# Kernel tuning notes

Measured on AMD Instinct MI355X. Metric: run time of the kernel, lower is better.

## Reference

```python
import jax, jax.numpy as jnp
import numpy as np

EPS = 1e-5


def _adabin_act_quant_1bit(x):
    # AdabinQuantizer, num_bits=1, layerwise=False, beta=0 (fresh zeros param).
    # alpha: per-sample scale, detached: 2*mean|x - beta| / sqrt(Qp=1), shape (N,1,1,1)
    alpha = jax.lax.stop_gradient(2.0 * jnp.mean(jnp.abs(x), axis=(1, 2, 3), keepdims=True))
    alpha = jnp.maximum(alpha, EPS)
    # forward: alpha * sign(x); STE grad: pass-through where |x/alpha| <= 1 (clip grad)
    clipped = jnp.clip(x / alpha, -1.0, 1.0)
    return alpha * (clipped + jax.lax.stop_gradient(jnp.sign(x) - clipped))


def _bwn_weight_quant(w):
    # BwnQuantizer, layerwise=False: per-output-channel L1 mean scale,
    # w_q = sign(w) * m, STE backward = identity.
    m = jnp.mean(jnp.abs(w), axis=(1, 2, 3), keepdims=True)  # (O,1,1,1)
    return w + jax.lax.stop_gradient(jnp.sign(w) * m - w)


def setup_inputs() -> dict:
    key = jax.random.key(0)
    kx, kw = jax.random.split(key)
    x = jax.random.normal(kx, (32, 256, 56, 56), dtype=jnp.float32)
    weight = jax.random.normal(kw, (256, 256, 3, 3), dtype=jnp.float32) * 0.05
    return {"x": x, "weight": weight}


def reference(x, weight):
    xq = _adabin_act_quant_1bit(x)
    wq = _bwn_weight_quant(weight)
    out = jax.lax.conv_general_dilated(
        xq, wq,
        window_strides=(1, 1),
        padding=((1, 1), (1, 1)),
        dimension_numbers=("NCHW", "OIHW", "NCHW"),
    )
    return out
```

## Files before the change

kernel.cpp:

```cpp
#include <hip/hip_runtime.h>
#include <cstdint>

typedef int   i32x4 __attribute__((ext_vector_type(4)));
typedef int   i32x8 __attribute__((ext_vector_type(8)));
typedef float f32x4 __attribute__((ext_vector_type(4)));

static constexpr int N_IMG = 32, HWP = 3136, KK = 2304, HP = 58;
static constexpr size_t XPAD_BYTES = (size_t)N_IMG * HP * HP * 256;
static constexpr size_t OFF_XPAD = 0;
static constexpr size_t OFF_WSGN = XPAD_BYTES;
static constexpr size_t OFF_MSC  = OFF_WSGN + (size_t)256 * KK;
static constexpr size_t OFF_ACC  = OFF_MSC + 1024;

__device__ __forceinline__ void async16(const void* g, const void* l) {
    __builtin_amdgcn_global_load_lds(
        (const __attribute__((address_space(1))) uint32_t*)g,
        (__attribute__((address_space(3))) uint32_t*)l, 16, 0, 0);
}

__device__ __forceinline__ unsigned char sign_fp8(float v) {
    return (v > 0.f) ? 0x38u : ((v < 0.f) ? 0xB8u : 0u);
}

__device__ __forceinline__ int xoff(int kt) {
    int rs = kt >> 1, rr = rs / 3, ss = rs - rr * 3;
    return (rr * HP + ss) * 256 + ((kt & 1) << 7);
}

__global__ __launch_bounds__(256) void k_wm(const float* __restrict__ w,
                                            unsigned char* __restrict__ wA,
                                            float* __restrict__ msc,
                                            float* __restrict__ acc32) {
    int ko = blockIdx.x, t = threadIdx.x;
    __shared__ unsigned char s[2304];
    __shared__ float red[4];
    float sum = 0.f;
    #pragma unroll
    for (int i = 0; i < 9; ++i) {
        float v = w[(size_t)ko * KK + i * 256 + t];
        sum += fabsf(v);
        s[i * 256 + t] = sign_fp8(v);
    }
    #pragma unroll
    for (int off = 32; off; off >>= 1) sum += __shfl_down(sum, off, 64);
    if ((t & 63) == 0) red[t >> 6] = sum;
    __syncthreads();
    if (t == 0) msc[ko] = (red[0] + red[1] + red[2] + red[3]) * (1.f / 2304.f);
    if (ko == 0 && t < 32) acc32[t] = 0.f;
    #pragma unroll
    for (int i = 0; i < 9; ++i)
        wA[((size_t)(i * 2 + (t >> 7)) * 256 + ko) * 128 + (t & 127)] = s[t * 9 + i];
}

__global__ __launch_bounds__(256) void k_xpad(const float* __restrict__ x,
                                              unsigned char* __restrict__ xpad,
                                              float* __restrict__ acc32) {
    int bx = blockIdx.x, n = blockIdx.y;
    int t = threadIdx.x;
    {
        int g = (n * 49 + bx) * 256 + t;
        if (g < 32 * 228 * 16) {
            int n2 = g / 3648, rem = g - n2 * 3648;
            int pos = rem >> 4, j = rem & 15;
            int h, wq;
            if (pos < 58)       { h = 0;         wq = pos; }
            else if (pos < 116) { h = 57;        wq = pos - 58; }
            else if (pos < 172) { h = pos - 115; wq = 0; }
            else                { h = pos - 171; wq = 57; }
            *(i32x4*)&xpad[(((size_t)n2 * HP + h) * HP + wq) * 256 + j * 16] =
                (i32x4){0, 0, 0, 0};
        }
    }
    int hw0 = bx * 64;
    int cg = t & 15, hwg = t >> 4;
    int c16 = cg * 16;
    int hwb = hw0 + hwg * 4;

    f32x4 v[16];
    #pragma unroll
    for (int jc = 0; jc < 16; ++jc)
        v[jc] = *(const f32x4*)&x[((size_t)(n * 256 + c16 + jc)) * HWP + hwb];

    float asum = 0.f;
    #pragma unroll
    for (int jc = 0; jc < 16; ++jc)
        #pragma unroll
        for (int k = 0; k < 4; ++k) asum += fabsf(v[jc][k]);

    int h = hwb / 56, wp = hwb - h * 56;
    unsigned char* dst = &xpad[(((size_t)n * HP + h + 1) * HP + (wp + 1)) * 256 + c16];
    #pragma unroll
    for (int k = 0; k < 4; ++k) {
        i32x4 pk;
        #pragma unroll
        for (int q = 0; q < 4; ++q) {
            pk[q] = (int)((unsigned)sign_fp8(v[4 * q + 0][k])
                        | ((unsigned)sign_fp8(v[4 * q + 1][k]) << 8)
                        | ((unsigned)sign_fp8(v[4 * q + 2][k]) << 16)
                        | ((unsigned)sign_fp8(v[4 * q + 3][k]) << 24));
        }
        *(i32x4*)(dst + (size_t)k * 256) = pk;
    }

    #pragma unroll
    for (int off = 32; off; off >>= 1) asum += __shfl_down(asum, off, 64);
    __shared__ float red[4];
    if ((t & 63) == 0) red[t >> 6] = asum;
    __syncthreads();
    if (t == 0) atomicAdd(&acc32[n], red[0] + red[1] + red[2] + red[3]);
}

__global__ __launch_bounds__(256, 2) void k_gemm(const unsigned char* __restrict__ wA,
                                                 const unsigned char* __restrict__ xpad,
                                                 const float* __restrict__ acc32,
                                                 const float* __restrict__ msc,
                                                 float* __restrict__ out) {
    __shared__ __attribute__((aligned(16))) unsigned char Wt[256 * 128];
    __shared__ __attribute__((aligned(16))) unsigned char Xt[128 * 128];
    const int t = threadIdx.x;
    const int lane = t & 63, wv = t >> 6;
    const int ntile = blockIdx.x;
    const int quad = lane >> 4, r16 = lane & 15;

    const int lrow = lane >> 3;
    const int pxs  = (lane & 7) ^ lrow;
    const int kc   = ((pxs & 3) << 1) | (pxs >> 2);

    const unsigned char* wp[8];
    unsigned char* ldsW[8];
    #pragma unroll
    for (int rnd = 0; rnd < 8; ++rnd) {
        int s = wv * 8 + rnd;
        int row = s * 8 + lrow;
        wp[rnd] = wA + (size_t)row * 128 + kc * 16;
        ldsW[rnd] = Wt + s * 1024;
    }
    const unsigned char* xp[4];
    unsigned char* ldsX[4];
    #pragma unroll
    for (int rnd = 0; rnd < 4; ++rnd) {
        int s = wv * 4 + rnd;
        int row = s * 8 + lrow;
        int p = ntile * 128 + row;
        int nimg = p / HWP, hw = p - nimg * HWP;
        int h = hw / 56, wpos = hw - h * 56;
        xp[rnd] = xpad + (((size_t)nimg * HP + h) * HP + wpos) * 256 + kc * 16;
        ldsX[rnd] = Xt + s * 1024;
    }

    f32x4 acc[4][8];
    #pragma unroll
    for (int i = 0; i < 4; ++i)
        #pragma unroll
        for (int j = 0; j < 8; ++j)
            acc[i][j] = (f32x4){0.f, 0.f, 0.f, 0.f};

    for (int kt = 0; kt < 18; ++kt) {
        const size_t offW = (size_t)kt * 32768;
        const int offX = xoff(kt);
        #pragma unroll
        for (int rnd = 0; rnd < 8; ++rnd) async16(wp[rnd] + offW, ldsW[rnd]);
        #pragma unroll
        for (int rnd = 0; rnd < 4; ++rnd) async16(xp[rnd] + offX, ldsX[rnd]);
        asm volatile("s_waitcnt vmcnt(0)" ::: "memory");
        __syncthreads();

        i32x8 a8[4];
        #pragma unroll
        for (int i = 0; i < 4; ++i) {
            int row = wv * 64 + i * 16 + r16, sw = row & 7;
            i32x4 lo = *(const i32x4*)(Wt + row * 128 + ((quad ^ sw) << 4));
            i32x4 hi = *(const i32x4*)(Wt + row * 128 + (((quad | 4) ^ sw) << 4));
            a8[i] = __builtin_shufflevector(lo, hi, 0, 1, 2, 3, 4, 5, 6, 7);
        }
        #pragma unroll
        for (int j = 0; j < 8; ++j) {
            int row = j * 16 + r16, sw = row & 7;
            i32x4 lo = *(const i32x4*)(Xt + row * 128 + ((quad ^ sw) << 4));
            i32x4 hi = *(const i32x4*)(Xt + row * 128 + (((quad | 4) ^ sw) << 4));
            i32x8 b8 = __builtin_shufflevector(lo, hi, 0, 1, 2, 3, 4, 5, 6, 7);
            #pragma unroll
            for (int i = 0; i < 4; ++i)
                acc[i][j] = __builtin_amdgcn_mfma_scale_f32_16x16x128_f8f6f4(
                    a8[i], b8, acc[i][j], 0, 0, 0, 127, 0, 127);
        }
        __syncthreads();
    }

    float mscv[4][4];
    #pragma unroll
    for (int i = 0; i < 4; ++i) {
        int ko0 = wv * 64 + i * 16 + quad * 4;
        #pragma unroll
        for (int r = 0; r < 4; ++r) mscv[i][r] = msc[ko0 + r];
    }
    #pragma unroll
    for (int j = 0; j < 8; ++j) {
        int p = ntile * 128 + j * 16 + r16;
        int nimg = p / HWP, hw = p - nimg * HWP;
        float av = fmaxf(acc32[nimg] * (2.f / 802816.f), 1e-5f);
        float* outp = out + (size_t)nimg * 802816 + hw;
        #pragma unroll
        for (int i = 0; i < 4; ++i) {
            int ko0 = wv * 64 + i * 16 + quad * 4;
            #pragma unroll
            for (int r = 0; r < 4; ++r)
                outp[(size_t)(ko0 + r) * HWP] = acc[i][j][r] * av * mscv[i][r];
        }
    }
}

extern "C" void kernel_launch(void* const* d_in, const int* in_sizes, int n_in,
                              void* d_out, int out_size, void* d_ws, size_t ws_size,
                              hipStream_t stream) {
    const float* x = (const float*)d_in[0];
    const float* w = (const float*)d_in[1];
    float* out = (float*)d_out;
    char* ws = (char*)d_ws;
    unsigned char* xpad = (unsigned char*)(ws + OFF_XPAD);
    unsigned char* wA   = (unsigned char*)(ws + OFF_WSGN);
    float* msc   = (float*)(ws + OFF_MSC);
    float* acc32 = (float*)(ws + OFF_ACC);

    k_wm<<<256, 256, 0, stream>>>(w, wA, msc, acc32);
    k_xpad<<<dim3(49, N_IMG), 256, 0, stream>>>(x, xpad, acc32);
    k_gemm<<<784, 256, 0, stream>>>(wA, xpad, acc32, msc, out);
}
```

Before: 250.8 us.

## Double-buffer LDS tiles in fp8 GEMM to prefetch next K-step during MFMA

Switches the GEMM kernel to a 96KB dynamic LDS allocation holding two stages of weight and activation tiles. The next K-step's async global-to-LDS loads are issued before computing on the current buffer, and the wait is deferred to the end of the iteration. This hides load latency within a block, but halves the intended occupancy to one block per CU, which gives up the overlap previously supplied by a co-resident block.

```diff
diff --git a/kernel.cpp b/kernel.cpp
--- a/kernel.cpp
+++ b/kernel.cpp
@@ -110,13 +110,12 @@
     if (t == 0) atomicAdd(&acc32[n], red[0] + red[1] + red[2] + red[3]);
 }
 
-__global__ __launch_bounds__(256, 2) void k_gemm(const unsigned char* __restrict__ wA,
+__global__ __launch_bounds__(256, 1) void k_gemm(const unsigned char* __restrict__ wA,
                                                  const unsigned char* __restrict__ xpad,
                                                  const float* __restrict__ acc32,
                                                  const float* __restrict__ msc,
                                                  float* __restrict__ out) {
-    __shared__ __attribute__((aligned(16))) unsigned char Wt[256 * 128];
-    __shared__ __attribute__((aligned(16))) unsigned char Xt[128 * 128];
+    extern __shared__ __attribute__((aligned(16))) unsigned char smem[];
     const int t = threadIdx.x;
     const int lane = t & 63, wv = t >> 6;
     const int ntile = blockIdx.x;
@@ -127,16 +126,16 @@
     const int kc   = ((pxs & 3) << 1) | (pxs >> 2);
 
     const unsigned char* wp[8];
-    unsigned char* ldsW[8];
+    int ldsWoff[8];
     #pragma unroll
     for (int rnd = 0; rnd < 8; ++rnd) {
         int s = wv * 8 + rnd;
         int row = s * 8 + lrow;
         wp[rnd] = wA + (size_t)row * 128 + kc * 16;
-        ldsW[rnd] = Wt + s * 1024;
+        ldsWoff[rnd] = s * 1024;
     }
     const unsigned char* xp[4];
-    unsigned char* ldsX[4];
+    int ldsXoff[4];
     #pragma unroll
     for (int rnd = 0; rnd < 4; ++rnd) {
         int s = wv * 4 + rnd;
@@ -145,7 +144,7 @@
         int nimg = p / HWP, hw = p - nimg * HWP;
         int h = hw / 56, wpos = hw - h * 56;
         xp[rnd] = xpad + (((size_t)nimg * HP + h) * HP + wpos) * 256 + kc * 16;
-        ldsX[rnd] = Xt + s * 1024;
+        ldsXoff[rnd] = 32768 + s * 1024;
     }
 
     f32x4 acc[4][8];
@@ -155,16 +154,31 @@
         for (int j = 0; j < 8; ++j)
             acc[i][j] = (f32x4){0.f, 0.f, 0.f, 0.f};
 
-    for (int kt = 0; kt < 18; ++kt) {
-        const size_t offW = (size_t)kt * 32768;
-        const int offX = xoff(kt);
-        #pragma unroll
-        for (int rnd = 0; rnd < 8; ++rnd) async16(wp[rnd] + offW, ldsW[rnd]);
-        #pragma unroll
-        for (int rnd = 0; rnd < 4; ++rnd) async16(xp[rnd] + offX, ldsX[rnd]);
+    {
+        const size_t offW = 0;
+        const int offX = xoff(0);
+        #pragma unroll
+        for (int rnd = 0; rnd < 8; ++rnd) async16(wp[rnd] + offW, smem + ldsWoff[rnd]);
+        #pragma unroll
+        for (int rnd = 0; rnd < 4; ++rnd) async16(xp[rnd] + offX, smem + ldsXoff[rnd]);
         asm volatile("s_waitcnt vmcnt(0)" ::: "memory");
         __syncthreads();
-
+    }
+
+    for (int kt = 0; kt < 18; ++kt) {
+        unsigned char* cb = smem + (size_t)(kt & 1) * 49152;
+        if (kt < 17) {
+            unsigned char* nb = smem + (size_t)((kt & 1) ^ 1) * 49152;
+            const size_t offW = (size_t)(kt + 1) * 32768;
+            const int offX = xoff(kt + 1);
+            #pragma unroll
+            for (int rnd = 0; rnd < 8; ++rnd) async16(wp[rnd] + offW, nb + ldsWoff[rnd]);
+            #pragma unroll
+            for (int rnd = 0; rnd < 4; ++rnd) async16(xp[rnd] + offX, nb + ldsXoff[rnd]);
+        }
+
+        const unsigned char* Wt = cb;
+        const unsigned char* Xt = cb + 32768;
         i32x8 a8[4];
         #pragma unroll
         for (int i = 0; i < 4; ++i) {
@@ -184,6 +198,8 @@
                 acc[i][j] = __builtin_amdgcn_mfma_scale_f32_16x16x128_f8f6f4(
                     a8[i], b8, acc[i][j], 0, 0, 0, 127, 0, 127);
         }
+
+        asm volatile("s_waitcnt vmcnt(0)" ::: "memory");
         __syncthreads();
     }
 
@@ -222,7 +238,14 @@
     float* msc   = (float*)(ws + OFF_MSC);
     float* acc32 = (float*)(ws + OFF_ACC);
 
+    static bool lds_opt_in = false;
+    if (!lds_opt_in) {
+        hipFuncSetAttribute((const void*)k_gemm,
+                            hipFuncAttributeMaxDynamicSharedMemorySize, 98304);
+        lds_opt_in = true;
+    }
+
     k_wm<<<256, 256, 0, stream>>>(w, wA, msc, acc32);
     k_xpad<<<dim3(49, N_IMG), 256, 0, stream>>>(x, xpad, acc32);
-    k_gemm<<<784, 256, 0, stream>>>(wA, xpad, acc32, msc, out);
-}
+    k_gemm<<<784, 256, 98304, stream>>>(wA, xpad, acc32, msc, out);
+}
```

Result: slower. 274.5 us (+9.4%).

## Pack sign operands as FP4 to halve activation and weight footprint

Applied to the files above, without the earlier changes.

Encodes activation and weight signs as 4-bit FP4 (E2M1, ±1.0) instead of FP8, halving the padded activation buffer and the sign weight matrix. The GEMM now walks 9 K-tiles of 256 channels instead of 18 tiles of 128, and issues two FP4 MFMAs per tile with zero-padded operands and a permuted LDS read pattern. The aim is to cut global and LDS traffic and the number of loop iterations. The cost is that each 16x16x128 MFMA uses only half of its operand width, so the number of MFMA instructions stays the same.

```diff
diff --git a/kernel.cpp b/kernel.cpp
--- a/kernel.cpp
+++ b/kernel.cpp
@@ -1,15 +1,16 @@
 #include <hip/hip_runtime.h>
 #include <cstdint>
 
-typedef int   i32x4 __attribute__((ext_vector_type(4)));
-typedef int   i32x8 __attribute__((ext_vector_type(8)));
-typedef float f32x4 __attribute__((ext_vector_type(4)));
+typedef int      i32x4 __attribute__((ext_vector_type(4)));
+typedef int      i32x8 __attribute__((ext_vector_type(8)));
+typedef float    f32x4 __attribute__((ext_vector_type(4)));
+typedef unsigned u32x2 __attribute__((ext_vector_type(2)));
 
 static constexpr int N_IMG = 32, HWP = 3136, KK = 2304, HP = 58;
-static constexpr size_t XPAD_BYTES = (size_t)N_IMG * HP * HP * 256;
+static constexpr size_t XPAD_BYTES = (size_t)N_IMG * HP * HP * 128;
 static constexpr size_t OFF_XPAD = 0;
 static constexpr size_t OFF_WSGN = XPAD_BYTES;
-static constexpr size_t OFF_MSC  = OFF_WSGN + (size_t)256 * KK;
+static constexpr size_t OFF_MSC  = OFF_WSGN + (size_t)9 * 256 * 128;
 static constexpr size_t OFF_ACC  = OFF_MSC + 1024;
 
 __device__ __forceinline__ void async16(const void* g, const void* l) {
@@ -18,13 +19,12 @@
         (__attribute__((address_space(3))) uint32_t*)l, 16, 0, 0);
 }
 
-__device__ __forceinline__ unsigned char sign_fp8(float v) {
-    return (v > 0.f) ? 0x38u : ((v < 0.f) ? 0xB8u : 0u);
-}
-
-__device__ __forceinline__ int xoff(int kt) {
-    int rs = kt >> 1, rr = rs / 3, ss = rs - rr * 3;
-    return (rr * HP + ss) * 256 + ((kt & 1) << 7);
+__device__ __forceinline__ unsigned sgn4(float v) {
+    return (v > 0.f) ? 0x2u : ((v < 0.f) ? 0xAu : 0u);
+}
+
+__device__ __forceinline__ i32x8 pad8(i32x4 v) {
+    return __builtin_shufflevector(v, (i32x4){0, 0, 0, 0}, 0, 1, 2, 3, 4, 5, 6, 7);
 }
 
 __global__ __launch_bounds__(256) void k_wm(const float* __restrict__ w,
@@ -39,7 +39,7 @@
     for (int i = 0; i < 9; ++i) {
         float v = w[(size_t)ko * KK + i * 256 + t];
         sum += fabsf(v);
-        s[i * 256 + t] = sign_fp8(v);
+        s[i * 256 + t] = (unsigned char)sgn4(v);
     }
     #pragma unroll
     for (int off = 32; off; off >>= 1) sum += __shfl_down(sum, off, 64);
@@ -47,9 +47,13 @@
     __syncthreads();
     if (t == 0) msc[ko] = (red[0] + red[1] + red[2] + red[3]) * (1.f / 2304.f);
     if (ko == 0 && t < 32) acc32[t] = 0.f;
-    #pragma unroll
-    for (int i = 0; i < 9; ++i)
-        wA[((size_t)(i * 2 + (t >> 7)) * 256 + ko) * 128 + (t & 127)] = s[t * 9 + i];
+    if (t < 128) {
+        #pragma unroll
+        for (int i = 0; i < 9; ++i) {
+            unsigned char b = (unsigned char)(s[(2 * t) * 9 + i] | (s[(2 * t + 1) * 9 + i] << 4));
+            wA[((size_t)i * 256 + ko) * 128 + t] = b;
+        }
+    }
 }
 
 __global__ __launch_bounds__(256) void k_xpad(const float* __restrict__ x,
@@ -59,15 +63,15 @@
     int t = threadIdx.x;
     {
         int g = (n * 49 + bx) * 256 + t;
-        if (g < 32 * 228 * 16) {
-            int n2 = g / 3648, rem = g - n2 * 3648;
-            int pos = rem >> 4, j = rem & 15;
+        if (g < 32 * 228 * 8) {
+            int n2 = g / 1824, rem = g - n2 * 1824;
+            int pos = rem >> 3, j = rem & 7;
             int h, wq;
             if (pos < 58)       { h = 0;         wq = pos; }
             else if (pos < 116) { h = 57;        wq = pos - 58; }
             else if (pos < 172) { h = pos - 115; wq = 0; }
             else                { h = pos - 171; wq = 57; }
-            *(i32x4*)&xpad[(((size_t)n2 * HP + h) * HP + wq) * 256 + j * 16] =
+            *(i32x4*)&xpad[(((size_t)n2 * HP + h) * HP + wq) * 128 + j * 16] =
                 (i32x4){0, 0, 0, 0};
         }
     }
@@ -88,18 +92,15 @@
         for (int k = 0; k < 4; ++k) asum += fabsf(v[jc][k]);
 
     int h = hwb / 56, wp = hwb - h * 56;
-    unsigned char* dst = &xpad[(((size_t)n * HP + h + 1) * HP + (wp + 1)) * 256 + c16];
+    unsigned char* dst = &xpad[(((size_t)n * HP + h + 1) * HP + (wp + 1)) * 128 + cg * 8];
     #pragma unroll
     for (int k = 0; k < 4; ++k) {
-        i32x4 pk;
-        #pragma unroll
-        for (int q = 0; q < 4; ++q) {
-            pk[q] = (int)((unsigned)sign_fp8(v[4 * q + 0][k])
-                        | ((unsigned)sign_fp8(v[4 * q + 1][k]) << 8)
-                        | ((unsigned)sign_fp8(v[4 * q + 2][k]) << 16)
-                        | ((unsigned)sign_fp8(v[4 * q + 3][k]) << 24));
-        }
-        *(i32x4*)(dst + (size_t)k * 256) = pk;
+        unsigned lo = 0, hi = 0;
+        #pragma unroll
+        for (int j = 0; j < 8; ++j) lo |= sgn4(v[j][k]) << (4 * j);
+        #pragma unroll
+        for (int j = 0; j < 8; ++j) hi |= sgn4(v[8 + j][k]) << (4 * j);
+        *(u32x2*)(dst + (size_t)k * 128) = (u32x2){lo, hi};
     }
 
     #pragma unroll
@@ -125,6 +126,8 @@
     const int lrow = lane >> 3;
     const int pxs  = (lane & 7) ^ lrow;
     const int kc   = ((pxs & 3) << 1) | (pxs >> 2);
+    const int pq  = (quad >> 1) | ((quad & 1) << 2);
+    const int pq4 = pq ^ 2;
 
     const unsigned char* wp[8];
     unsigned char* ldsW[8];
@@ -144,7 +147,7 @@
         int p = ntile * 128 + row;
         int nimg = p / HWP, hw = p - nimg * HWP;
         int h = hw / 56, wpos = hw - h * 56;
-        xp[rnd] = xpad + (((size_t)nimg * HP + h) * HP + wpos) * 256 + kc * 16;
+        xp[rnd] = xpad + (((size_t)nimg * HP + h) * HP + wpos) * 128 + kc * 16;
         ldsX[rnd] = Xt + s * 1024;
     }
 
@@ -155,9 +158,10 @@
         for (int j = 0; j < 8; ++j)
             acc[i][j] = (f32x4){0.f, 0.f, 0.f, 0.f};
 
-    for (int kt = 0; kt < 18; ++kt) {
-        const size_t offW = (size_t)kt * 32768;
-        const int offX = xoff(kt);
+    for (int rs = 0; rs < 9; ++rs) {
+        const int rr = rs / 3, ss = rs - rr * 3;
+        const size_t offW = (size_t)rs * 32768;
+        const int offX = (rr * HP + ss) * 128;
         #pragma unroll
         for (int rnd = 0; rnd < 8; ++rnd) async16(wp[rnd] + offW, ldsW[rnd]);
         #pragma unroll
@@ -165,24 +169,27 @@
         asm volatile("s_waitcnt vmcnt(0)" ::: "memory");
         __syncthreads();
 
-        i32x8 a8[4];
+        i32x4 alo[4], ahi[4];
         #pragma unroll
         for (int i = 0; i < 4; ++i) {
             int row = wv * 64 + i * 16 + r16, sw = row & 7;
-            i32x4 lo = *(const i32x4*)(Wt + row * 128 + ((quad ^ sw) << 4));
-            i32x4 hi = *(const i32x4*)(Wt + row * 128 + (((quad | 4) ^ sw) << 4));
-            a8[i] = __builtin_shufflevector(lo, hi, 0, 1, 2, 3, 4, 5, 6, 7);
+            alo[i] = *(const i32x4*)(Wt + row * 128 + ((pq ^ sw) << 4));
+            ahi[i] = *(const i32x4*)(Wt + row * 128 + ((pq4 ^ sw) << 4));
         }
         #pragma unroll
         for (int j = 0; j < 8; ++j) {
             int row = j * 16 + r16, sw = row & 7;
-            i32x4 lo = *(const i32x4*)(Xt + row * 128 + ((quad ^ sw) << 4));
-            i32x4 hi = *(const i32x4*)(Xt + row * 128 + (((quad | 4) ^ sw) << 4));
-            i32x8 b8 = __builtin_shufflevector(lo, hi, 0, 1, 2, 3, 4, 5, 6, 7);
+            i32x4 blo = *(const i32x4*)(Xt + row * 128 + ((pq ^ sw) << 4));
+            i32x4 bhi = *(const i32x4*)(Xt + row * 128 + ((pq4 ^ sw) << 4));
+            i32x8 bl8 = pad8(blo), bh8 = pad8(bhi);
             #pragma unroll
             for (int i = 0; i < 4; ++i)
                 acc[i][j] = __builtin_amdgcn_mfma_scale_f32_16x16x128_f8f6f4(
-                    a8[i], b8, acc[i][j], 0, 0, 0, 127, 0, 127);
+                    pad8(alo[i]), bl8, acc[i][j], 4, 4, 0, 127, 0, 127);
+            #pragma unroll
+            for (int i = 0; i < 4; ++i)
+                acc[i][j] = __builtin_amdgcn_mfma_scale_f32_16x16x128_f8f6f4(
+                    pad8(ahi[i]), bh8, acc[i][j], 4, 4, 0, 127, 0, 127);
         }
         __syncthreads();
     }
```

Result: faster. 226.6 us (-9.7%).
